# Performance work log

Hardware: AMD Instinct MI355X
Metric: run time of the kernel (lower is better)

## Reference

```python
import jax, jax.numpy as jnp
import numpy as np

B, T, N, S = 128, 1024, 128, 256
NEG = jnp.float32(-1e30)  # acts as -inf but keeps grads finite


def setup_inputs() -> dict:
    key = jax.random.key(0)
    k1, k2, k3, k4, k5 = jax.random.split(key, 5)
    inputs = jax.random.normal(k1, (B, T, N), dtype=jnp.float32)
    # nn.Parameter inits to zeros; use small noise so transition actually participates
    transition = 0.05 * jax.random.normal(k2, (N, N), dtype=jnp.float32)
    targets = jax.random.randint(k3, (B, S), 0, N)
    input_lengths = jax.random.randint(k4, (B,), T // 2, T + 1).astype(jnp.int32)
    target_lengths = jax.random.randint(k5, (B,), S // 2, S + 1).astype(jnp.int32)
    return {
        "transition": transition,
        "inputs": inputs,
        "targets": targets,
        "input_lengths": input_lengths,
        "target_lengths": target_lengths,
    }


def reference(transition, inputs, targets, input_lengths, target_lengths):
    # ASG loss = FCC (free-running partition) - FAC (forced alignment score),
    # scale_mode='none', reduction='mean'. transition[j, i] = score of label i -> j.
    xs = jnp.moveaxis(inputs, 1, 0)  # (T, B, N)
    ts = jnp.arange(1, T)

    # ---- FCC: alpha[t, b, j] = x[t,b,j] + logsumexp_i(alpha[t-1,b,i] + trans[j,i])
    def fcc_step(alpha, xt):
        x_t, t = xt
        new = x_t + jax.nn.logsumexp(alpha[:, None, :] + transition[None, :, :], axis=-1)
        return jnp.where((t < input_lengths)[:, None], new, alpha), None

    alphaT, _ = jax.lax.scan(fcc_step, xs[0], (xs[1:], ts))
    fcc = jax.nn.logsumexp(alphaT, axis=-1)  # (B,)

    # ---- FAC: beta[t, b, s] over target positions, self/next transitions only
    self_tr = transition[targets, targets]  # (B, S): stay on targets[s]
    prev_lbl = jnp.concatenate([targets[:, :1], targets[:, :-1]], axis=1)
    next_tr = transition[targets, prev_lbl]  # (B, S): targets[s-1] -> targets[s]

    em0 = jnp.take_along_axis(xs[0], targets, axis=1)  # (B, S)
    beta0 = jnp.where(jnp.arange(S)[None, :] == 0, em0, NEG)

    def fac_step(beta, xt):
        x_t, t = xt
        em = jnp.take_along_axis(x_t, targets, axis=1)  # (B, S)
        shifted = jnp.concatenate(
            [jnp.full((B, 1), NEG, dtype=beta.dtype), beta[:, :-1]], axis=1
        )
        new = em + jnp.logaddexp(beta + self_tr, shifted + next_tr)
        return jnp.where((t < input_lengths)[:, None], new, beta), None

    betaT, _ = jax.lax.scan(fac_step, beta0, (xs[1:], ts))
    fac = jnp.take_along_axis(betaT, (target_lengths - 1)[:, None], axis=1)[:, 0]

    return jnp.mean(fcc - fac)
```

## Files before the change

kernel.cpp:

```cpp
#include <hip/hip_runtime.h>
#include <hip/hip_bf16.h>

#define Bb 128
#define Tt 1024
#define Nn 128
#define Ss 256
#define NEGF (-1e30f)
#define D9 9.0f

typedef __attribute__((ext_vector_type(8))) short short8;
typedef __attribute__((ext_vector_type(4))) float f32x4;

__device__ __forceinline__ short bf16b(float f) {
    __hip_bfloat16 h = __float2bfloat16(f);
    return *reinterpret_cast<short*>(&h);
}

#define FCC_STEP(t_, k_)                                                       \
    {                                                                          \
        const int t = (t_);                                                    \
        if ((k_) == 0) { \
            float m = fmaxf(fmaxf(wred[0][g], wred[1][g]),                     \
                            fmaxf(wred[2][g], wred[3][g]));                    \
            if (t < len) {                                                     \
                float invm = 1.0f / m;                                         \
                wc[0][0] *= invm; wc[0][1] *= invm;                            \
                wc[0][2] *= invm; wc[0][3] *= invm;                            \
                wc[1][0] *= invm; wc[1][1] *= invm;                            \
                wc[1][2] *= invm; wc[1][3] *= invm;                            \
                c += __logf(m);                                                \
            }                                                                  \
        }                                                                      \
        const short* up = &ut[(t - 1) & 1][g][0] + quad * 8;                   \
        short8 bf0 = *(const short8*)(up);                                     \
        short8 bf1 = *(const short8*)(up + 32);                                \
        short8 bf2 = *(const short8*)(up + 64);                                \
        short8 bf3 = *(const short8*)(up + 96);                                \
        f32x4 a0p = {0.f, 0.f, 0.f, 0.f}, a0q = {0.f, 0.f, 0.f, 0.f};          \
        f32x4 a1p = {0.f, 0.f, 0.f, 0.f}, a1q = {0.f, 0.f, 0.f, 0.f};          \
        a0p = __builtin_amdgcn_mfma_f32_16x16x32_bf16(ea[0][0], bf0, a0p, 0, 0, 0); \
        a1p = __builtin_amdgcn_mfma_f32_16x16x32_bf16(ea[1][0], bf0, a1p, 0, 0, 0); \
        a0q = __builtin_amdgcn_mfma_f32_16x16x32_bf16(ea[0][2], bf2, a0q, 0, 0, 0); \
        a1q = __builtin_amdgcn_mfma_f32_16x16x32_bf16(ea[1][2], bf2, a1q, 0, 0, 0); \
        a0p = __builtin_amdgcn_mfma_f32_16x16x32_bf16(ea[0][1], bf1, a0p, 0, 0, 0); \
        a1p = __builtin_amdgcn_mfma_f32_16x16x32_bf16(ea[1][1], bf1, a1p, 0, 0, 0); \
        a0q = __builtin_amdgcn_mfma_f32_16x16x32_bf16(ea[0][3], bf3, a0q, 0, 0, 0); \
        a1q = __builtin_amdgcn_mfma_f32_16x16x32_bf16(ea[1][3], bf3, a1q, 0, 0, 0); \
        const bool act = (t < len);                                            \
        float un[2][4];                                                        \
        un[0][0] = act ? wc[0][0] * (a0p[0] + a0q[0]) : uprev[0][0];           \
        un[0][1] = act ? wc[0][1] * (a0p[1] + a0q[1]) : uprev[0][1];           \
        un[0][2] = act ? wc[0][2] * (a0p[2] + a0q[2]) : uprev[0][2];           \
        un[0][3] = act ? wc[0][3] * (a0p[3] + a0q[3]) : uprev[0][3];           \
        un[1][0] = act ? wc[1][0] * (a1p[0] + a1q[0]) : uprev[1][0];           \
        un[1][1] = act ? wc[1][1] * (a1p[1] + a1q[1]) : uprev[1][1];           \
        un[1][2] = act ? wc[1][2] * (a1p[2] + a1q[2]) : uprev[1][2];           \
        un[1][3] = act ? wc[1][3] * (a1p[3] + a1q[3]) : uprev[1][3];           \
        uprev[0][0] = un[0][0]; uprev[0][1] = un[0][1];                        \
        uprev[0][2] = un[0][2]; uprev[0][3] = un[0][3];                        \
        uprev[1][0] = un[1][0]; uprev[1][1] = un[1][1];                        \
        uprev[1][2] = un[1][2]; uprev[1][3] = un[1][3];                        \
        {                                                                      \
            short4 s4;                                                         \
            s4.x = bf16b(un[0][0]); s4.y = bf16b(un[0][1]);                    \
            s4.z = bf16b(un[0][2]); s4.w = bf16b(un[0][3]);                    \
            *reinterpret_cast<short4*>(&ut[t & 1][g][j0_]) = s4;               \
            s4.x = bf16b(un[1][0]); s4.y = bf16b(un[1][1]);                    \
            s4.z = bf16b(un[1][2]); s4.w = bf16b(un[1][3]);                    \
            *reinterpret_cast<short4*>(&ut[t & 1][g][j0_ + 16]) = s4;          \
        }                                                                      \
               \
        const int sl = ((k_) + 1) & 3;                                         \
        wc[0][0] = __expf(xs[sl][0].x - D9);                                   \
        wc[0][1] = __expf(xs[sl][0].y - D9);                                   \
        wc[0][2] = __expf(xs[sl][0].z - D9);                                   \
        wc[0][3] = __expf(xs[sl][0].w - D9);                                   \
        wc[1][0] = __expf(xs[sl][1].x - D9);                                   \
        wc[1][1] = __expf(xs[sl][1].y - D9);                                   \
        wc[1][2] = __expf(xs[sl][1].z - D9);                                   \
        wc[1][3] = __expf(xs[sl][1].w - D9);                                   \
             \
                       \
        {                                                                      \
            int kk = t + 5; if (kk > Tt - 1) kk = Tt - 1;                      \
            xs[sl][0] = *(const float4*)(xb + (size_t)kk * Nn + j0_);          \
            xs[sl][1] = *(const float4*)(xb + (size_t)kk * Nn + j0_ + 16);     \
        }                                                                      \
        if ((k_) == 7) {                                   \
            float mm = un[0][0];                                               \
            mm = fmaxf(mm, un[0][1]); mm = fmaxf(mm, un[0][2]);                \
            mm = fmaxf(mm, un[0][3]); mm = fmaxf(mm, un[1][0]);                \
            mm = fmaxf(mm, un[1][1]); mm = fmaxf(mm, un[1][2]);                \
            mm = fmaxf(mm, un[1][3]);                                          \
            mm = fmaxf(mm, __shfl_xor(mm, 16));                                \
            mm = fmaxf(mm, __shfl_xor(mm, 32));                                \
            if (lane < 16) wred[q][lane] = mm;                                 \
        }                                                                      \
        __syncthreads();                                                       \
    }

#define FAC_STEP(t_, k_)                                                       \
    {                                                                          \
        const int t = (t_);                                                    \
        const int d = ((k_) + 7) & 7;                                          \
        float e0 = em[d][0], e1 = em[d][1], e2 = em[d][2], e3 = em[d][3];      \
        int tn = t + 8; if (tn > Tt - 1) tn = Tt - 1;                          \
        const float* xrow = xb + (size_t)tn * Nn;                              \
        em[d][0] = xrow[tgi[0]]; em[d][1] = xrow[tgi[1]];                      \
        em[d][2] = xrow[tgi[2]]; em[d][3] = xrow[tgi[3]];                      \
        float bup = __shfl_up(bt[3], 1);                                       \
        float prev0 = (lane == 0) ? NEGF : bup;                                \
        float nb[4];                                                           \
        {                                                                      \
            float aa = bt[0] + st[0], bb = prev0 + ntr[0];                     \
            float hi = fmaxf(aa, bb), lo = fminf(aa, bb);                      \
            nb[0] = e0 + hi + __logf(1.0f + __expf(lo - hi));                  \
        }                                                                      \
        {                                                                      \
            float aa = bt[1] + st[1], bb = bt[0] + ntr[1];                     \
            float hi = fmaxf(aa, bb), lo = fminf(aa, bb);                      \
            nb[1] = e1 + hi + __logf(1.0f + __expf(lo - hi));                  \
        }                                                                      \
        {                                                                      \
            float aa = bt[2] + st[2], bb = bt[1] + ntr[2];                     \
            float hi = fmaxf(aa, bb), lo = fminf(aa, bb);                      \
            nb[2] = e2 + hi + __logf(1.0f + __expf(lo - hi));                  \
        }                                                                      \
        {                                                                      \
            float aa = bt[3] + st[3], bb = bt[2] + ntr[3];                     \
            float hi = fmaxf(aa, bb), lo = fminf(aa, bb);                      \
            nb[3] = e3 + hi + __logf(1.0f + __expf(lo - hi));                  \
        }                                                                      \
        if (t < len) {                                                         \
            bt[0] = nb[0]; bt[1] = nb[1]; bt[2] = nb[2]; bt[3] = nb[3];        \
        }                                                                      \
    }

__global__ __launch_bounds__(256) void asg_main(
    const float* __restrict__ trans, const float* __restrict__ x,
    const int* __restrict__ targets, const int* __restrict__ ilen,
    const int* __restrict__ tlen,
    float* __restrict__ fcc_out, float* __restrict__ fac_out)
{
    __shared__ __align__(16) short ut[2][16][136];
    __shared__ float wred[4][16];

    const int tid  = threadIdx.x;
    const int q    = tid >> 6;
    const int lane = tid & 63;
    const int g    = lane & 15;
    const int quad = lane >> 4;

    if (blockIdx.x < 8) {
        const int b   = (blockIdx.x << 4) + g;
        const int len = ilen[b];
        const float* xb = x + (size_t)b * Tt * Nn;

        short8 ea[2][4];
        #pragma unroll
        for (int mt = 0; mt < 2; ++mt) {
            const float* tr = trans + (size_t)(32 * q + 16 * mt + g) * Nn + quad * 8;
            #pragma unroll
            for (int kc = 0; kc < 4; ++kc) {
                short8 v;
                #pragma unroll
                for (int jj = 0; jj < 8; ++jj)
                    v[jj] = bf16b(__expf(tr[kc * 32 + jj]));
                ea[mt][kc] = v;
            }
        }

        const int j0_ = 32 * q + 4 * quad;

        float uprev[2][4];
        #pragma unroll
        for (int mt = 0; mt < 2; ++mt) {
            const int j0 = j0_ + 16 * mt;
            float4 xv = *(const float4*)(xb + j0);
            uprev[mt][0] = __expf(xv.x); uprev[mt][1] = __expf(xv.y);
            uprev[mt][2] = __expf(xv.z); uprev[mt][3] = __expf(xv.w);
            short4 s4;
            s4.x = bf16b(uprev[mt][0]); s4.y = bf16b(uprev[mt][1]);
            s4.z = bf16b(uprev[mt][2]); s4.w = bf16b(uprev[mt][3]);
            *reinterpret_cast<short4*>(&ut[0][g][j0]) = s4;
        }

        float wc[2][4];
        float4 xs[4][2];
        #pragma unroll
        for (int mt = 0; mt < 2; ++mt) {
            const int j0 = j0_ + 16 * mt;
            float4 xv = *(const float4*)(xb + Nn + j0);
            wc[mt][0] = __expf(xv.x - D9); wc[mt][1] = __expf(xv.y - D9);
            wc[mt][2] = __expf(xv.z - D9); wc[mt][3] = __expf(xv.w - D9);
            #pragma unroll
            for (int k = 2; k <= 5; ++k)
                xs[k & 3][mt] = *(const float4*)(xb + (size_t)k * Nn + j0);
        }
        float c = 0.0f;
        __syncthreads();

        #pragma unroll
        for (int k = 1; k < 8; ++k) FCC_STEP(k, k)
        for (int tb = 8; tb < Tt; tb += 8) {
            #pragma unroll
            for (int k = 0; k < 8; ++k) FCC_STEP(tb + k, k)
        }

        c += D9 * (float)(len - 1);

        float s = 0.f;
        #pragma unroll
        for (int mt = 0; mt < 2; ++mt)
            #pragma unroll
            for (int r = 0; r < 4; ++r) s += uprev[mt][r];
        s += __shfl_xor(s, 16);
        s += __shfl_xor(s, 32);
        if (lane < 16) wred[q][lane] = s;
        __syncthreads();
        if (tid < 16) {
            float tot = wred[0][tid] + wred[1][tid] + wred[2][tid] + wred[3][tid];
            fcc_out[(blockIdx.x << 4) + tid] = c + __logf(tot);
        }
    } else {
        const int b   = ((blockIdx.x - 8) << 2) + q;
        const int len = ilen[b];
        const int tl  = tlen[b];
        const float* xb = x + (size_t)b * Tt * Nn;

        int   tgi[4];
        float st[4], ntr[4], bt[4];
        #pragma unroll
        for (int r = 0; r < 4; ++r) {
            const int s = (lane << 2) + r;
            const int tgv = targets[b * Ss + s];
            const int pg  = (s == 0) ? tgv : targets[b * Ss + s - 1];
            tgi[r] = tgv;
            st[r]  = trans[tgv * Nn + tgv];
            ntr[r] = trans[tgv * Nn + pg];
            bt[r]  = (s == 0) ? xb[tgv] : NEGF;
        }
        float em[8][4];
        #pragma unroll
        for (int k = 1; k <= 8; ++k) {
            int tt = k; if (tt > Tt - 1) tt = Tt - 1;
            const float* xrow = xb + (size_t)tt * Nn;
            em[(k - 1) & 7][0] = xrow[tgi[0]];
            em[(k - 1) & 7][1] = xrow[tgi[1]];
            em[(k - 1) & 7][2] = xrow[tgi[2]];
            em[(k - 1) & 7][3] = xrow[tgi[3]];
        }

        #pragma unroll
        for (int k = 1; k < 8; ++k) FAC_STEP(k, k)
        for (int tb = 8; tb < Tt; tb += 8) {
            #pragma unroll
            for (int k = 0; k < 8; ++k) FAC_STEP(tb + k, k)
        }

        #pragma unroll
        for (int r = 0; r < 4; ++r)
            if ((lane << 2) + r == tl - 1) fac_out[b] = bt[r];
    }
}

__global__ __launch_bounds__(128) void reduce_kernel(const float* __restrict__ fcc,
                                                     const float* __restrict__ fac,
                                                     float* __restrict__ out) {
    __shared__ float r2[2];
    int tid = threadIdx.x;
    float v = fcc[tid] - fac[tid];
    #pragma unroll
    for (int o = 32; o > 0; o >>= 1) v += __shfl_xor(v, o);
    if ((tid & 63) == 0) r2[tid >> 6] = v;
    __syncthreads();
    if (tid == 0) out[0] = (r2[0] + r2[1]) * (1.0f / Bb);
}

extern "C" void kernel_launch(void* const* d_in, const int* in_sizes, int n_in,
                              void* d_out, int out_size, void* d_ws, size_t ws_size,
                              hipStream_t stream) {
    const float* trans   = (const float*)d_in[0];
    const float* x       = (const float*)d_in[1];
    const int*   targets = (const int*)d_in[2];
    const int*   ilen    = (const int*)d_in[3];
    const int*   tlen    = (const int*)d_in[4];
    float* out = (float*)d_out;

    float* fcc = (float*)d_ws;
    float* fac = fcc + Bb;

    asg_main<<<8 + Bb / 4, 256, 0, stream>>>(trans, x, targets, ilen, tlen, fcc, fac);
    reduce_kernel<<<1, 128, 0, stream>>>(fcc, fac, out);
}
```

Baseline: 392.2 us.

## Pack two FCC batch groups per block and drop per-step length masking

The FCC part now runs two 16-batch groups per 512-thread block, and the FAC part runs eight batches per block, so the grid shrinks from 40 blocks to 20. The per-step `t < len` select is removed. Instead, wave 0 computes the alpha sum with an extra ones-vector MFMA each step and latches it, together with the log-scale, when t equals the batch's input length. The transition rows are permuted so each lane writes eight contiguous bf16 values with one int4 store, and the two MFMA accumulator chains per tile are merged into one. This trades the per-step select for extra MFMAs on wave 0 and a longer accumulate dependency, and each barrier now spans eight waves instead of four.

```diff
diff --git a/kernel.cpp b/kernel.cpp
--- a/kernel.cpp
+++ b/kernel.cpp
@@ -15,86 +15,71 @@
     __hip_bfloat16 h = __float2bfloat16(f);
     return *reinterpret_cast<short*>(&h);
 }
+__device__ __forceinline__ int pk2(float lo, float hi) {
+    return (int)(((unsigned int)(unsigned short)bf16b(lo)) |
+                 ((unsigned int)(unsigned short)bf16b(hi) << 16));
+}
+
+#define MFMA16(A, B, C) __builtin_amdgcn_mfma_f32_16x16x32_bf16((A), (B), (C), 0, 0, 0)
 
 #define FCC_STEP(t_, k_)                                                       \
     {                                                                          \
         const int t = (t_);                                                    \
-        if ((k_) == 0) { \
-            float m = fmaxf(fmaxf(wred[0][g], wred[1][g]),                     \
-                            fmaxf(wred[2][g], wred[3][g]));                    \
-            if (t < len) {                                                     \
-                float invm = 1.0f / m;                                         \
-                wc[0][0] *= invm; wc[0][1] *= invm;                            \
-                wc[0][2] *= invm; wc[0][3] *= invm;                            \
-                wc[1][0] *= invm; wc[1][1] *= invm;                            \
-                wc[1][2] *= invm; wc[1][3] *= invm;                            \
-                c += __logf(m);                                                \
-            }                                                                  \
-        }                                                                      \
-        const short* up = &ut[(t - 1) & 1][g][0] + quad * 8;                   \
-        short8 bf0 = *(const short8*)(up);                                     \
-        short8 bf1 = *(const short8*)(up + 32);                                \
-        short8 bf2 = *(const short8*)(up + 64);                                \
-        short8 bf3 = *(const short8*)(up + 96);                                \
-        f32x4 a0p = {0.f, 0.f, 0.f, 0.f}, a0q = {0.f, 0.f, 0.f, 0.f};          \
-        f32x4 a1p = {0.f, 0.f, 0.f, 0.f}, a1q = {0.f, 0.f, 0.f, 0.f};          \
-        a0p = __builtin_amdgcn_mfma_f32_16x16x32_bf16(ea[0][0], bf0, a0p, 0, 0, 0); \
-        a1p = __builtin_amdgcn_mfma_f32_16x16x32_bf16(ea[1][0], bf0, a1p, 0, 0, 0); \
-        a0q = __builtin_amdgcn_mfma_f32_16x16x32_bf16(ea[0][2], bf2, a0q, 0, 0, 0); \
-        a1q = __builtin_amdgcn_mfma_f32_16x16x32_bf16(ea[1][2], bf2, a1q, 0, 0, 0); \
-        a0p = __builtin_amdgcn_mfma_f32_16x16x32_bf16(ea[0][1], bf1, a0p, 0, 0, 0); \
-        a1p = __builtin_amdgcn_mfma_f32_16x16x32_bf16(ea[1][1], bf1, a1p, 0, 0, 0); \
-        a0q = __builtin_amdgcn_mfma_f32_16x16x32_bf16(ea[0][3], bf3, a0q, 0, 0, 0); \
-        a1q = __builtin_amdgcn_mfma_f32_16x16x32_bf16(ea[1][3], bf3, a1q, 0, 0, 0); \
-        const bool act = (t < len);                                            \
-        float un[2][4];                                                        \
-        un[0][0] = act ? wc[0][0] * (a0p[0] + a0q[0]) : uprev[0][0];           \
-        un[0][1] = act ? wc[0][1] * (a0p[1] + a0q[1]) : uprev[0][1];           \
-        un[0][2] = act ? wc[0][2] * (a0p[2] + a0q[2]) : uprev[0][2];           \
-        un[0][3] = act ? wc[0][3] * (a0p[3] + a0q[3]) : uprev[0][3];           \
-        un[1][0] = act ? wc[1][0] * (a1p[0] + a1q[0]) : uprev[1][0];           \
-        un[1][1] = act ? wc[1][1] * (a1p[1] + a1q[1]) : uprev[1][1];           \
-        un[1][2] = act ? wc[1][2] * (a1p[2] + a1q[2]) : uprev[1][2];           \
-        un[1][3] = act ? wc[1][3] * (a1p[3] + a1q[3]) : uprev[1][3];           \
-        uprev[0][0] = un[0][0]; uprev[0][1] = un[0][1];                        \
-        uprev[0][2] = un[0][2]; uprev[0][3] = un[0][3];                        \
-        uprev[1][0] = un[1][0]; uprev[1][1] = un[1][1];                        \
-        uprev[1][2] = un[1][2]; uprev[1][3] = un[1][3];                        \
-        {                                                                      \
-            short4 s4;                                                         \
-            s4.x = bf16b(un[0][0]); s4.y = bf16b(un[0][1]);                    \
-            s4.z = bf16b(un[0][2]); s4.w = bf16b(un[0][3]);                    \
-            *reinterpret_cast<short4*>(&ut[t & 1][g][j0_]) = s4;               \
-            s4.x = bf16b(un[1][0]); s4.y = bf16b(un[1][1]);                    \
-            s4.z = bf16b(un[1][2]); s4.w = bf16b(un[1][3]);                    \
-            *reinterpret_cast<short4*>(&ut[t & 1][g][j0_ + 16]) = s4;          \
-        }                                                                      \
-               \
+        float mren = 0.0f;                                                     \
+        if ((k_) == 0) {   \
+            mren = fmaxf(fmaxf(wredp[0][g], wredp[1][g]),                      \
+                         fmaxf(wredp[2][g], wredp[3][g]));                     \
+            float invm = 1.0f / mren;                                          \
+            wc[0] *= invm; wc[1] *= invm; wc[2] *= invm; wc[3] *= invm;        \
+            wc[4] *= invm; wc[5] *= invm; wc[6] *= invm; wc[7] *= invm;        \
+        }                                                                      \
+        const short* ub = ubuf[(t - 1) & 1] + g * 136 + quad * 8;              \
+        short8 bf0 = *(const short8*)(ub);                                     \
+        short8 bf1 = *(const short8*)(ub + 32);                                \
+        short8 bf2 = *(const short8*)(ub + 64);                                \
+        short8 bf3 = *(const short8*)(ub + 96);                                \
+        f32x4 a0 = {0.f, 0.f, 0.f, 0.f}, a1 = {0.f, 0.f, 0.f, 0.f};            \
+        a0 = MFMA16(ea[0][0], bf0, a0);  a1 = MFMA16(ea[1][0], bf0, a1);       \
+        a0 = MFMA16(ea[0][1], bf1, a0);  a1 = MFMA16(ea[1][1], bf1, a1);       \
+        a0 = MFMA16(ea[0][2], bf2, a0);  a1 = MFMA16(ea[1][2], bf2, a1);       \
+        a0 = MFMA16(ea[0][3], bf3, a0);  a1 = MFMA16(ea[1][3], bf3, a1);       \
+        if (q == 0) {  \
+            f32x4 aS = {0.f, 0.f, 0.f, 0.f};                                   \
+            aS = MFMA16(ones, bf0, aS);  aS = MFMA16(ones, bf1, aS);           \
+            aS = MFMA16(ones, bf2, aS);  aS = MFMA16(ones, bf3, aS);           \
+            if (t == leng) { Sreg = aS[0]; Creg = c; }                         \
+        }                                                                      \
+        if ((k_) == 0) c += __logf(mren);                                      \
+        float un[8];                                                           \
+        un[0] = wc[0] * a0[0]; un[1] = wc[1] * a0[1];                          \
+        un[2] = wc[2] * a0[2]; un[3] = wc[3] * a0[3];                          \
+        un[4] = wc[4] * a1[0]; un[5] = wc[5] * a1[1];                          \
+        un[6] = wc[6] * a1[2]; un[7] = wc[7] * a1[3];                          \
+        {                                                                      \
+            int4 dw;                                                           \
+            dw.x = pk2(un[0], un[1]); dw.y = pk2(un[2], un[3]);                \
+            dw.z = pk2(un[4], un[5]); dw.w = pk2(un[6], un[7]);                \
+            *(int4*)(ubuf[t & 1] + g * 136 + base) = dw;                       \
+        }                                                                      \
         const int sl = ((k_) + 1) & 3;                                         \
-        wc[0][0] = __expf(xs[sl][0].x - D9);                                   \
-        wc[0][1] = __expf(xs[sl][0].y - D9);                                   \
-        wc[0][2] = __expf(xs[sl][0].z - D9);                                   \
-        wc[0][3] = __expf(xs[sl][0].w - D9);                                   \
-        wc[1][0] = __expf(xs[sl][1].x - D9);                                   \
-        wc[1][1] = __expf(xs[sl][1].y - D9);                                   \
-        wc[1][2] = __expf(xs[sl][1].z - D9);                                   \
-        wc[1][3] = __expf(xs[sl][1].w - D9);                                   \
-             \
-                       \
+        wc[0] = __expf(xs[sl][0].x - D9); wc[1] = __expf(xs[sl][0].y - D9);    \
+        wc[2] = __expf(xs[sl][0].z - D9); wc[3] = __expf(xs[sl][0].w - D9);    \
+        wc[4] = __expf(xs[sl][1].x - D9); wc[5] = __expf(xs[sl][1].y - D9);    \
+        wc[6] = __expf(xs[sl][1].z - D9); wc[7] = __expf(xs[sl][1].w - D9);    \
         {                                                                      \
             int kk = t + 5; if (kk > Tt - 1) kk = Tt - 1;                      \
-            xs[sl][0] = *(const float4*)(xb + (size_t)kk * Nn + j0_);          \
-            xs[sl][1] = *(const float4*)(xb + (size_t)kk * Nn + j0_ + 16);     \
-        }                                                                      \
-        if ((k_) == 7) {                                   \
-            float mm = un[0][0];                                               \
-            mm = fmaxf(mm, un[0][1]); mm = fmaxf(mm, un[0][2]);                \
-            mm = fmaxf(mm, un[0][3]); mm = fmaxf(mm, un[1][0]);                \
-            mm = fmaxf(mm, un[1][1]); mm = fmaxf(mm, un[1][2]);                \
-            mm = fmaxf(mm, un[1][3]);                                          \
+            const float* xr_ = xb + (size_t)kk * Nn + base;                    \
+            xs[sl][0] = *(const float4*)(xr_);                                 \
+            xs[sl][1] = *(const float4*)(xr_ + 4);                             \
+        }                                                                      \
+        if ((k_) == 7) { \
+            float mm = un[0];                                                  \
+            mm = fmaxf(mm, un[1]); mm = fmaxf(mm, un[2]); mm = fmaxf(mm, un[3]); \
+            mm = fmaxf(mm, un[4]); mm = fmaxf(mm, un[5]); mm = fmaxf(mm, un[6]); \
+            mm = fmaxf(mm, un[7]);                                             \
             mm = fmaxf(mm, __shfl_xor(mm, 16));                                \
             mm = fmaxf(mm, __shfl_xor(mm, 32));                                \
-            if (lane < 16) wred[q][lane] = mm;                                 \
+            if (lane < 16) wredp[q][lane] = mm;                                \
         }                                                                      \
         __syncthreads();                                                       \
     }
@@ -136,68 +121,74 @@
         }                                                                      \
     }
 
-__global__ __launch_bounds__(256) void asg_main(
+__global__ __launch_bounds__(512, 2) void asg_main(
     const float* __restrict__ trans, const float* __restrict__ x,
     const int* __restrict__ targets, const int* __restrict__ ilen,
     const int* __restrict__ tlen,
     float* __restrict__ fcc_out, float* __restrict__ fac_out)
 {
-    __shared__ __align__(16) short ut[2][16][136];
-    __shared__ float wred[4][16];
+    __shared__ __align__(16) short uts[2][2][16][136];
+    __shared__ float wred[2][4][16];
 
     const int tid  = threadIdx.x;
-    const int q    = tid >> 6;
+    const int q8   = tid >> 6;
     const int lane = tid & 63;
-    const int g    = lane & 15;
-    const int quad = lane >> 4;
-
-    if (blockIdx.x < 8) {
-        const int b   = (blockIdx.x << 4) + g;
-        const int len = ilen[b];
+
+    if (blockIdx.x < 4) {
+        const int grp  = q8 >> 2;
+        const int q    = q8 & 3;
+        const int g    = lane & 15;
+        const int quad = lane >> 4;
+        const int base = 32 * q + 8 * quad;
+        const int group = (blockIdx.x << 1) + grp;
+        const int b    = group * 16 + g;
+        const int leng = ilen[b];
         const float* xb = x + (size_t)b * Tt * Nn;
 
+        short* ubuf[2] = { &uts[grp][0][0][0], &uts[grp][1][0][0] };
+        float (*wredp)[16] = wred[grp];
+
         short8 ea[2][4];
         #pragma unroll
         for (int mt = 0; mt < 2; ++mt) {
-            const float* tr = trans + (size_t)(32 * q + 16 * mt + g) * Nn + quad * 8;
+            const int jr = 32 * q + 8 * (g >> 2) + 4 * mt + (g & 3);
+            const float* tr = trans + (size_t)jr * Nn + quad * 8;
             #pragma unroll
             for (int kc = 0; kc < 4; ++kc) {
                 short8 v;
                 #pragma unroll
-                for (int jj = 0; jj < 8; ++jj)
-                    v[jj] = bf16b(__expf(tr[kc * 32 + jj]));
+                for (int jj = 0; jj < 8; ++jj) v[jj] = bf16b(__expf(tr[kc * 32 + jj]));
                 ea[mt][kc] = v;
             }
         }
-
-        const int j0_ = 32 * q + 4 * quad;
-
-        float uprev[2][4];
-        #pragma unroll
-        for (int mt = 0; mt < 2; ++mt) {
-            const int j0 = j0_ + 16 * mt;
-            float4 xv = *(const float4*)(xb + j0);
-            uprev[mt][0] = __expf(xv.x); uprev[mt][1] = __expf(xv.y);
-            uprev[mt][2] = __expf(xv.z); uprev[mt][3] = __expf(xv.w);
-            short4 s4;
-            s4.x = bf16b(uprev[mt][0]); s4.y = bf16b(uprev[mt][1]);
-            s4.z = bf16b(uprev[mt][2]); s4.w = bf16b(uprev[mt][3]);
-            *reinterpret_cast<short4*>(&ut[0][g][j0]) = s4;
-        }
-
-        float wc[2][4];
+        short8 ones;
+        #pragma unroll
+        for (int jj = 0; jj < 8; ++jj) ones[jj] = (short)0x3F80;
+
+        {
+            const float* x0 = xb + base;
+            int4 dw;
+            dw.x = pk2(__expf(x0[0]), __expf(x0[1]));
+            dw.y = pk2(__expf(x0[2]), __expf(x0[3]));
+            dw.z = pk2(__expf(x0[4]), __expf(x0[5]));
+            dw.w = pk2(__expf(x0[6]), __expf(x0[7]));
+            *(int4*)(ubuf[0] + g * 136 + base) = dw;
+        }
+
+        float wc[8];
         float4 xs[4][2];
-        #pragma unroll
-        for (int mt = 0; mt < 2; ++mt) {
-            const int j0 = j0_ + 16 * mt;
-            float4 xv = *(const float4*)(xb + Nn + j0);
-            wc[mt][0] = __expf(xv.x - D9); wc[mt][1] = __expf(xv.y - D9);
-            wc[mt][2] = __expf(xv.z - D9); wc[mt][3] = __expf(xv.w - D9);
-            #pragma unroll
-            for (int k = 2; k <= 5; ++k)
-                xs[k & 3][mt] = *(const float4*)(xb + (size_t)k * Nn + j0);
-        }
-        float c = 0.0f;
+        {
+            const float* x1 = xb + Nn + base;
+            #pragma unroll
+            for (int i = 0; i < 8; ++i) wc[i] = __expf(x1[i] - D9);
+            #pragma unroll
+            for (int k = 2; k <= 5; ++k) {
+                const float* xr_ = xb + (size_t)k * Nn + base;
+                xs[k & 3][0] = *(const float4*)(xr_);
+                xs[k & 3][1] = *(const float4*)(xr_ + 4);
+            }
+        }
+        float c = 0.0f, Sreg = 1.0f, Creg = 0.0f;
         __syncthreads();
 
         #pragma unroll
@@ -207,23 +198,21 @@
             for (int k = 0; k < 8; ++k) FCC_STEP(tb + k, k)
         }
 
-        c += D9 * (float)(len - 1);
-
-        float s = 0.f;
-        #pragma unroll
-        for (int mt = 0; mt < 2; ++mt)
-            #pragma unroll
-            for (int r = 0; r < 4; ++r) s += uprev[mt][r];
-        s += __shfl_xor(s, 16);
-        s += __shfl_xor(s, 32);
-        if (lane < 16) wred[q][lane] = s;
-        __syncthreads();
-        if (tid < 16) {
-            float tot = wred[0][tid] + wred[1][tid] + wred[2][tid] + wred[3][tid];
-            fcc_out[(blockIdx.x << 4) + tid] = c + __logf(tot);
+        if (q == 0) {
+            const short* ub = ubuf[1] + g * 136 + quad * 8;
+            short8 bf0 = *(const short8*)(ub);
+            short8 bf1 = *(const short8*)(ub + 32);
+            short8 bf2 = *(const short8*)(ub + 64);
+            short8 bf3 = *(const short8*)(ub + 96);
+            f32x4 aS = {0.f, 0.f, 0.f, 0.f};
+            aS = MFMA16(ones, bf0, aS);  aS = MFMA16(ones, bf1, aS);
+            aS = MFMA16(ones, bf2, aS);  aS = MFMA16(ones, bf3, aS);
+            if (leng == Tt) { Sreg = aS[0]; Creg = c; }
+            if (quad == 0)
+                fcc_out[b] = Creg + __logf(Sreg) + D9 * (float)(leng - 1);
         }
     } else {
-        const int b   = ((blockIdx.x - 8) << 2) + q;
+        const int b   = ((blockIdx.x - 4) << 3) + q8;
         const int len = ilen[b];
         const int tl  = tlen[b];
         const float* xb = x + (size_t)b * Tt * Nn;
@@ -250,14 +239,12 @@
             em[(k - 1) & 7][2] = xrow[tgi[2]];
             em[(k - 1) & 7][3] = xrow[tgi[3]];
         }
-
         #pragma unroll
         for (int k = 1; k < 8; ++k) FAC_STEP(k, k)
         for (int tb = 8; tb < Tt; tb += 8) {
             #pragma unroll
             for (int k = 0; k < 8; ++k) FAC_STEP(tb + k, k)
         }
-
         #pragma unroll
         for (int r = 0; r < 4; ++r)
             if ((lane << 2) + r == tl - 1) fac_out[b] = bt[r];
@@ -290,6 +277,6 @@
     float* fcc = (float*)d_ws;
     float* fac = fcc + Bb;
 
-    asg_main<<<8 + Bb / 4, 256, 0, stream>>>(trans, x, targets, ilen, tlen, fcc, fac);
+    asg_main<<<20, 512, 0, stream>>>(trans, x, targets, ilen, tlen, fcc, fac);
     reduce_kernel<<<1, 128, 0, stream>>>(fcc, fac, out);
 }
```

New measurement: 547.2 us. 1.4x slower.
